# Optimization experiments

Hardware: AMD Instinct MI355X
Metric: run time of the kernel (lower is better)

## Reference

```python
import jax, jax.numpy as jnp
import numpy as np

R_MAX = 2.0
DR_MIN = 0.02
N_ATOMS = 200000
N_EDGES = 12800000

def setup_inputs() -> dict:
    key = jax.random.key(0)
    k1, k2, k3, k4, k5, k6 = jax.random.split(key, 6)
    R = jax.random.normal(k1, (N_ATOMS, 3), dtype=jnp.float32)
    dr_vec = jax.random.normal(k2, (N_EDGES, 3), dtype=jnp.float32)
    Z = jax.random.randint(k3, (N_ATOMS,), 0, 119, dtype=jnp.int32)
    idx = jax.random.randint(k4, (2, N_EDGES), 0, N_ATOMS, dtype=jnp.int32)
    box = jnp.zeros((3, 3), dtype=jnp.float32)
    rep_scale = jax.random.uniform(k5, (119,), dtype=jnp.float32, minval=0.2, maxval=1.8)
    rep_prefactor = jax.random.uniform(k6, (119,), dtype=jnp.float32, minval=0.5, maxval=2.0)
    return {"R": R, "dr_vec": dr_vec, "Z": Z, "idx": idx, "box": box,
            "properties": 0, "rep_scale": rep_scale, "rep_prefactor": rep_prefactor}

def reference(R, dr_vec, Z, idx, box, properties, rep_scale, rep_prefactor):
    idx_i, idx_j = idx[0], idx[1]
    # gather per-edge atomic numbers, then per-element parameters
    Z_i = Z[idx_i]
    Z_j = Z[idx_j]
    # per-edge distance, clipped to [0.02, r_max]
    dr = jnp.sqrt(jnp.sum(dr_vec * dr_vec, axis=-1)).astype(jnp.float32)
    dr = jnp.clip(dr, 0.02, R_MAX)
    cos_cutoff = 0.5 * (jnp.cos(np.pi * dr / R_MAX) + 1.0)
    A_i = jnp.abs(rep_prefactor[Z_i])
    A_j = jnp.abs(rep_prefactor[Z_j])
    R_i = jnp.abs(rep_scale[Z_i])
    R_j = jnp.abs(rep_scale[Z_j])
    f = A_i * A_j * jnp.exp(-dr * (R_i + R_j) / (R_i * R_j)) / (dr * dr)
    E_ij = f * cos_cutoff
    # mask padding/self edges (apax pads neighbor lists with idx_i == idx_j)
    mask = (idx_i != idx_j).astype(E_ij.dtype)
    E_ij = E_ij * mask
    # fp64_sum in original; high-precision accumulation via plain sum here
    E = jnp.sum(E_ij)
    return E
```

## Files before the change

### kernel.cpp

```cpp
#include <hip/hip_runtime.h>
#include <hip/hip_bf16.h>

#define RMAXF 2.0f
#define PI_F 3.14159265358979f


__global__ __launch_bounds__(256) void edge_kernel(
    const float4* __restrict__ dr4,
    const int*    __restrict__ idx_i,
    const int*    __restrict__ idx_j,
    const int*    __restrict__ Z,
    const float*  __restrict__ rep_scale,
    const float*  __restrict__ rep_prefactor,
    float*        __restrict__ out,
    int n_quads, int n_edges)
{
    __shared__ float2 tab[128];
    for (int t = threadIdx.x; t < 119; t += blockDim.x)
        tab[t] = make_float2(fabsf(rep_prefactor[t]), fabsf(rep_scale[t]));
    __syncthreads();

    float acc = 0.0f;
    const int stride = gridDim.x * blockDim.x;

    for (int q = blockIdx.x * blockDim.x + threadIdx.x; q < n_quads; q += stride) {
        float4 a = dr4[3 * q + 0];
        float4 b = dr4[3 * q + 1];
        float4 c = dr4[3 * q + 2];
        int4 i4 = ((const int4*)idx_i)[q];
        int4 j4 = ((const int4*)idx_j)[q];

        float d2[4];
        d2[0] = a.x * a.x + a.y * a.y + a.z * a.z;
        d2[1] = a.w * a.w + b.x * b.x + b.y * b.y;
        d2[2] = b.z * b.z + b.w * b.w + c.x * c.x;
        d2[3] = c.y * c.y + c.z * c.z + c.w * c.w;

        int ii[4] = { i4.x, i4.y, i4.z, i4.w };
        int jj[4] = { j4.x, j4.y, j4.z, j4.w };

        int zi[4], zj[4];
        #pragma unroll
        for (int k = 0; k < 4; ++k) { zi[k] = Z[ii[k]]; zj[k] = Z[jj[k]]; }

        #pragma unroll
        for (int k = 0; k < 4; ++k) {
            float dr = __builtin_amdgcn_sqrtf(d2[k]);
            dr = fminf(fmaxf(dr, 0.02f), RMAXF);
            float cc = 0.5f * (__cosf((PI_F / RMAXF) * dr) + 1.0f);
            float2 pi_ = tab[zi[k]];
            float2 pj_ = tab[zj[k]];
            float inv_rr = __builtin_amdgcn_rcpf(pi_.y * pj_.y);
            float e  = __expf(-dr * (pi_.y + pj_.y) * inv_rr);
            float f  = pi_.x * pj_.x * e * __builtin_amdgcn_rcpf(dr * dr);
            f *= cc;
            acc += (ii[k] != jj[k]) ? f : 0.0f;
        }
    }

    if (blockIdx.x == 0 && threadIdx.x == 0) {
        const float* drf = (const float*)dr4;
        for (int e = n_quads * 4; e < n_edges; ++e) {
            float x = drf[3 * e + 0], y = drf[3 * e + 1], z = drf[3 * e + 2];
            float dr = sqrtf(x * x + y * y + z * z);
            dr = fminf(fmaxf(dr, 0.02f), RMAXF);
            float cc = 0.5f * (__cosf((PI_F / RMAXF) * dr) + 1.0f);
            int i = idx_i[e], j = idx_j[e];
            float2 pi_ = tab[Z[i]];
            float2 pj_ = tab[Z[j]];
            float e_ = __expf(-dr * (pi_.y + pj_.y) / (pi_.y * pj_.y));
            float f  = pi_.x * pj_.x * e_ / (dr * dr) * cc;
            if (i != j) acc += f;
        }
    }

    #pragma unroll
    for (int off = 32; off > 0; off >>= 1)
        acc += __shfl_down(acc, off, 64);

    __shared__ float wsum[4];
    int lane = threadIdx.x & 63;
    int wid  = threadIdx.x >> 6;
    if (lane == 0) wsum[wid] = acc;
    __syncthreads();
    if (threadIdx.x == 0) {
        float s = wsum[0] + wsum[1] + wsum[2] + wsum[3];
        atomicAdd(out, s);
    }
}

extern "C" void kernel_launch(void* const* d_in, const int* in_sizes, int n_in,
                              void* d_out, int out_size, void* d_ws, size_t ws_size,
                              hipStream_t stream) {
    const float* dr_vec        = (const float*)d_in[1];
    const int*   Z             = (const int*)d_in[2];
    const int*   idx           = (const int*)d_in[3];
    const float* rep_scale     = (const float*)d_in[6];
    const float* rep_prefactor = (const float*)d_in[7];
    float* out = (float*)d_out;

    const int n_edges = in_sizes[3] / 2;
    const int n_quads = n_edges / 4;
    const int* idx_i = idx;
    const int* idx_j = idx + n_edges;

    hipMemsetAsync(d_out, 0, sizeof(float), stream);

    int blocks = (n_quads + 255) / 256;
    if (blocks > 2048) blocks = 2048;
    edge_kernel<<<blocks, 256, 0, stream>>>(
        (const float4*)dr_vec, idx_i, idx_j, Z, rep_scale, rep_prefactor,
        out, n_quads, n_edges);
}
```

Before: 356.2 us.

## Precompute per-atom params in workspace, simplify edge math, launch one quad per thread

Adds a pre-pass that builds a per-atom (|A|, 1/|R|) float2 table in workspace, so each edge does one 8-byte gather per endpoint instead of a Z gather followed by an LDS table lookup. The edge formula is rewritten algebraically: the exponent uses the sum of inverse scales, the clamp is applied to d², and the cosine cutoff becomes cos²(pi·dr/4), which removes a reciprocal and some arithmetic. The grid-stride loop is replaced by one quad per thread with many more blocks, which means more block-level atomics, and a fallback kernel covers unaligned edge counts or insufficient workspace. The pre-pass adds an extra launch and a 1.6 MB write.

```diff
diff --git a/kernel.cpp b/kernel.cpp
--- a/kernel.cpp
+++ b/kernel.cpp
@@ -4,31 +4,46 @@
 #define RMAXF 2.0f
 #define PI_F 3.14159265358979f
 
+__global__ __launch_bounds__(256) void build_params(
+    const int*   __restrict__ Z,
+    const float* __restrict__ rep_scale,
+    const float* __restrict__ rep_prefactor,
+    float2*      __restrict__ par,
+    int n_atoms)
+{
+    int a = blockIdx.x * blockDim.x + threadIdx.x;
+    if (a < n_atoms) {
+        int z = Z[a];
+        float A = fabsf(rep_prefactor[z]);
+        float S = __builtin_amdgcn_rcpf(fabsf(rep_scale[z]));
+        par[a] = make_float2(A, S);
+    }
+}
 
 __global__ __launch_bounds__(256) void edge_kernel(
     const float4* __restrict__ dr4,
-    const int*    __restrict__ idx_i,
-    const int*    __restrict__ idx_j,
-    const int*    __restrict__ Z,
-    const float*  __restrict__ rep_scale,
-    const float*  __restrict__ rep_prefactor,
+    const int4*   __restrict__ idx_i4,
+    const int4*   __restrict__ idx_j4,
+    const float2* __restrict__ par,
     float*        __restrict__ out,
     int n_quads, int n_edges)
 {
-    __shared__ float2 tab[128];
-    for (int t = threadIdx.x; t < 119; t += blockDim.x)
-        tab[t] = make_float2(fabsf(rep_prefactor[t]), fabsf(rep_scale[t]));
-    __syncthreads();
+    int q = blockIdx.x * blockDim.x + threadIdx.x;
+    float acc = 0.0f;
 
-    float acc = 0.0f;
-    const int stride = gridDim.x * blockDim.x;
-
-    for (int q = blockIdx.x * blockDim.x + threadIdx.x; q < n_quads; q += stride) {
+    if (q < n_quads) {
         float4 a = dr4[3 * q + 0];
         float4 b = dr4[3 * q + 1];
         float4 c = dr4[3 * q + 2];
-        int4 i4 = ((const int4*)idx_i)[q];
-        int4 j4 = ((const int4*)idx_j)[q];
+        int4 i4 = idx_i4[q];
+        int4 j4 = idx_j4[q];
+
+        int ii[4] = { i4.x, i4.y, i4.z, i4.w };
+        int jj[4] = { j4.x, j4.y, j4.z, j4.w };
+
+        float2 pi_[4], pj_[4];
+        #pragma unroll
+        for (int k = 0; k < 4; ++k) { pi_[k] = par[ii[k]]; pj_[k] = par[jj[k]]; }
 
         float d2[4];
         d2[0] = a.x * a.x + a.y * a.y + a.z * a.z;
@@ -36,40 +51,29 @@
         d2[2] = b.z * b.z + b.w * b.w + c.x * c.x;
         d2[3] = c.y * c.y + c.z * c.z + c.w * c.w;
 
-        int ii[4] = { i4.x, i4.y, i4.z, i4.w };
-        int jj[4] = { j4.x, j4.y, j4.z, j4.w };
-
-        int zi[4], zj[4];
-        #pragma unroll
-        for (int k = 0; k < 4; ++k) { zi[k] = Z[ii[k]]; zj[k] = Z[jj[k]]; }
-
         #pragma unroll
         for (int k = 0; k < 4; ++k) {
-            float dr = __builtin_amdgcn_sqrtf(d2[k]);
-            dr = fminf(fmaxf(dr, 0.02f), RMAXF);
-            float cc = 0.5f * (__cosf((PI_F / RMAXF) * dr) + 1.0f);
-            float2 pi_ = tab[zi[k]];
-            float2 pj_ = tab[zj[k]];
-            float inv_rr = __builtin_amdgcn_rcpf(pi_.y * pj_.y);
-            float e  = __expf(-dr * (pi_.y + pj_.y) * inv_rr);
-            float f  = pi_.x * pj_.x * e * __builtin_amdgcn_rcpf(dr * dr);
-            f *= cc;
+            float d2c = fminf(fmaxf(d2[k], 4.0e-4f), 4.0f);
+            float dr  = __builtin_amdgcn_sqrtf(d2c);
+            float cv  = __cosf((0.25f * PI_F) * dr);
+            float e   = __expf(-dr * (pi_[k].y + pj_[k].y));
+            float f   = pi_[k].x * pj_[k].x * e * __builtin_amdgcn_rcpf(d2c) * cv * cv;
             acc += (ii[k] != jj[k]) ? f : 0.0f;
         }
     }
 
-    if (blockIdx.x == 0 && threadIdx.x == 0) {
+    if (blockIdx.x == gridDim.x - 1 && threadIdx.x == 0) {
         const float* drf = (const float*)dr4;
+        const int* idx_i = (const int*)idx_i4;
+        const int* idx_j = (const int*)idx_j4;
         for (int e = n_quads * 4; e < n_edges; ++e) {
             float x = drf[3 * e + 0], y = drf[3 * e + 1], z = drf[3 * e + 2];
-            float dr = sqrtf(x * x + y * y + z * z);
-            dr = fminf(fmaxf(dr, 0.02f), RMAXF);
-            float cc = 0.5f * (__cosf((PI_F / RMAXF) * dr) + 1.0f);
+            float d2c = fminf(fmaxf(x * x + y * y + z * z, 4.0e-4f), 4.0f);
+            float dr  = sqrtf(d2c);
+            float cv  = __cosf((0.25f * PI_F) * dr);
             int i = idx_i[e], j = idx_j[e];
-            float2 pi_ = tab[Z[i]];
-            float2 pj_ = tab[Z[j]];
-            float e_ = __expf(-dr * (pi_.y + pj_.y) / (pi_.y * pj_.y));
-            float f  = pi_.x * pj_.x * e_ / (dr * dr) * cc;
+            float2 pi_ = par[i], pj_ = par[j];
+            float f = pi_.x * pj_.x * __expf(-dr * (pi_.y + pj_.y)) / d2c * cv * cv;
             if (i != j) acc += f;
         }
     }
@@ -83,10 +87,50 @@
     int wid  = threadIdx.x >> 6;
     if (lane == 0) wsum[wid] = acc;
     __syncthreads();
-    if (threadIdx.x == 0) {
-        float s = wsum[0] + wsum[1] + wsum[2] + wsum[3];
-        atomicAdd(out, s);
+    if (threadIdx.x == 0)
+        atomicAdd(out, wsum[0] + wsum[1] + wsum[2] + wsum[3]);
+}
+
+__global__ __launch_bounds__(256) void edge_kernel_fallback(
+    const float* __restrict__ drf,
+    const int*   __restrict__ idx_i,
+    const int*   __restrict__ idx_j,
+    const int*   __restrict__ Z,
+    const float* __restrict__ rep_scale,
+    const float* __restrict__ rep_prefactor,
+    float*       __restrict__ out,
+    int n_edges)
+{
+    __shared__ float2 tab[128];
+    for (int t = threadIdx.x; t < 119; t += blockDim.x)
+        tab[t] = make_float2(fabsf(rep_prefactor[t]),
+                             __builtin_amdgcn_rcpf(fabsf(rep_scale[t])));
+    __syncthreads();
+
+    float acc = 0.0f;
+    const int stride = gridDim.x * blockDim.x;
+    for (int e = blockIdx.x * blockDim.x + threadIdx.x; e < n_edges; e += stride) {
+        float x = drf[3 * e + 0], y = drf[3 * e + 1], z = drf[3 * e + 2];
+        float d2c = fminf(fmaxf(x * x + y * y + z * z, 4.0e-4f), 4.0f);
+        float dr  = __builtin_amdgcn_sqrtf(d2c);
+        float cv  = __cosf((0.25f * PI_F) * dr);
+        int i = idx_i[e], j = idx_j[e];
+        float2 pi_ = tab[Z[i]], pj_ = tab[Z[j]];
+        float f = pi_.x * pj_.x * __expf(-dr * (pi_.y + pj_.y))
+                  * __builtin_amdgcn_rcpf(d2c) * cv * cv;
+        acc += (i != j) ? f : 0.0f;
     }
+
+    #pragma unroll
+    for (int off = 32; off > 0; off >>= 1)
+        acc += __shfl_down(acc, off, 64);
+    __shared__ float wsum[4];
+    int lane = threadIdx.x & 63;
+    int wid  = threadIdx.x >> 6;
+    if (lane == 0) wsum[wid] = acc;
+    __syncthreads();
+    if (threadIdx.x == 0)
+        atomicAdd(out, wsum[0] + wsum[1] + wsum[2] + wsum[3]);
 }
 
 extern "C" void kernel_launch(void* const* d_in, const int* in_sizes, int n_in,
@@ -99,6 +143,7 @@
     const float* rep_prefactor = (const float*)d_in[7];
     float* out = (float*)d_out;
 
+    const int n_atoms = in_sizes[2];
     const int n_edges = in_sizes[3] / 2;
     const int n_quads = n_edges / 4;
     const int* idx_i = idx;
@@ -106,9 +151,20 @@
 
     hipMemsetAsync(d_out, 0, sizeof(float), stream);
 
-    int blocks = (n_quads + 255) / 256;
-    if (blocks > 2048) blocks = 2048;
-    edge_kernel<<<blocks, 256, 0, stream>>>(
-        (const float4*)dr_vec, idx_i, idx_j, Z, rep_scale, rep_prefactor,
-        out, n_quads, n_edges);
+    const size_t par_bytes = (size_t)n_atoms * sizeof(float2);
+    const bool aligned = ((n_edges & 3) == 0);
+
+    if (ws_size >= par_bytes && aligned) {
+        float2* par = (float2*)d_ws;
+        build_params<<<(n_atoms + 255) / 256, 256, 0, stream>>>(
+            Z, rep_scale, rep_prefactor, par, n_atoms);
+        edge_kernel<<<(n_quads + 255) / 256, 256, 0, stream>>>(
+            (const float4*)dr_vec, (const int4*)idx_i, (const int4*)idx_j,
+            par, out, n_quads, n_edges);
+    } else {
+        int blocks = (n_edges + 255) / 256;
+        if (blocks > 4096) blocks = 4096;
+        edge_kernel_fallback<<<blocks, 256, 0, stream>>>(
+            dr_vec, idx_i, idx_j, Z, rep_scale, rep_prefactor, out, n_edges);
+    }
 }
```

Result: slower. 385.3 us (+8.2%).
